# Kernel tuning notes

Measured on AMD Instinct MI355X. Metric: run time of the kernel, lower is better.

The kernel has to match this reference:

```python
import jax, jax.numpy as jnp
import numpy as np

INV_SQRT2 = 0.7071067811865476  # Haar (db1) filter coefficient


def haar_dwt(x):
    """Single-level Haar DWT along last axis (even length). Matches pywt db1."""
    e = x[..., 0::2]
    o = x[..., 1::2]
    ca = (e + o) * INV_SQRT2
    cd = (e - o) * INV_SQRT2
    return ca, cd


def haar_idwt(ca, cd):
    """Single-level Haar inverse DWT along last axis. Matches pywt waverec."""
    e = (ca + cd) * INV_SQRT2
    o = (ca - cd) * INV_SQRT2
    # interleave: out[2k]=e[k], out[2k+1]=o[k]
    return jnp.stack([e, o], axis=-1).reshape(ca.shape[:-1] + (2 * ca.shape[-1],))


def _soft_threshold(c, thr):
    a = jnp.abs(c)
    return jnp.where(a >= thr, jnp.sign(c) * (a - thr), jnp.zeros_like(c))


def setup_inputs() -> dict:
    key = jax.random.key(0)
    x = jax.random.normal(key, (64, 1024, 1024), dtype=jnp.float32)
    return {"x": x}


def reference(x):
    # x: [B, C, L]; 3-level Haar decomposition per (b, c) signal, vectorized.
    L = x.shape[-1]
    ca1, cd1 = haar_dwt(x)    # [B,C,L/2]
    ca2, cd2 = haar_dwt(ca1)  # [B,C,L/4]
    ca3, cd3 = haar_dwt(ca2)  # [B,C,L/8]

    # Universal threshold per signal: sigma = median(|cd1|)/0.6745,
    # lamda = sigma * sqrt(2*ln(L))  (natural log, as in math.log(L, e)).
    median_cd1 = jnp.median(jnp.abs(cd1), axis=-1, keepdims=True)  # [B,C,1]
    sigma = median_cd1 / 0.6745
    lamda = sigma * np.sqrt(2.0 * np.log(float(L))).astype(np.float32)

    # Per-level soft thresholds: lamda/log2(2), lamda/log2(3), lamda/log2(4).
    cd1 = _soft_threshold(cd1, lamda / np.float32(np.log2(2.0)))
    cd2 = _soft_threshold(cd2, lamda / np.float32(np.log2(3.0)))
    cd3 = _soft_threshold(cd3, lamda / np.float32(np.log2(4.0)))

    # Reconstruct with kept ca3 and thresholded details.
    ca2r = haar_idwt(ca3, cd3)
    ca1r = haar_idwt(ca2r, cd2)
    return haar_idwt(ca1r, cd1)
```

## Files before the change

### kernel.cpp

```cpp
#include <hip/hip_runtime.h>

#define L 1024
#define BLOCK 256

__device__ __forceinline__ float soft_thr(float c, float thr) {
    float a = fabsf(c);
    return (a >= thr) ? copysignf(a - thr, c) : 0.0f;
}

__device__ __forceinline__ int imin2(int a, int b) { return (a < b) ? a : b; }
__device__ __forceinline__ int imax2(int a, int b) { return (a > b) ? a : b; }

__global__ __launch_bounds__(BLOCK) void wavelet_denoise_kernel(
        const float* __restrict__ x, float* __restrict__ out) {
    constexpr float IS2 = 0.70710678118654752f;
    constexpr float SQRT_2LOGL = 3.7232974111f;

    const int lane = threadIdx.x & 63;
    const int wid  = threadIdx.x >> 6;
    const long long row = (long long)blockIdx.x * 4 + wid;
    const float* xr = x + row * L;
    float* orow = out + row * L;

    float4 in[4];
    #pragma unroll
    for (int j = 0; j < 4; ++j)
        in[j] = ((const float4*)xr)[j * 64 + lane];

    float ca1[8], cd1[8];
    #pragma unroll
    for (int j = 0; j < 4; ++j) {
        ca1[2*j]   = (in[j].x + in[j].y) * IS2;
        cd1[2*j]   = (in[j].x - in[j].y) * IS2;
        ca1[2*j+1] = (in[j].z + in[j].w) * IS2;
        cd1[2*j+1] = (in[j].z - in[j].w) * IS2;
    }

    float ca2[4], cd2[4];
    #pragma unroll
    for (int j = 0; j < 4; ++j) {
        ca2[j] = (ca1[2*j] + ca1[2*j+1]) * IS2;
        cd2[j] = (ca1[2*j] - ca1[2*j+1]) * IS2;
    }

    float ca3[4], cd3[4];
    #pragma unroll
    for (int j = 0; j < 4; ++j) {
        float o = __shfl_xor(ca2[j], 1);
        ca3[j] = (ca2[j] + o) * IS2;
        cd3[j] = (ca2[j] - o) * IS2;
    }

    int w[8];
    const int b0 = -(int)( lane       & 1);
    const int b1 = -(int)((lane >> 1) & 1);
    const int b2 = -(int)((lane >> 2) & 1);
    const int b3 = -(int)((lane >> 3) & 1);
    const int b4 = -(int)((lane >> 4) & 1);
    const int b5 = -(int)((lane >> 5) & 1);

    #pragma unroll
    for (int r = 0; r < 8; ++r)
        w[r] = (__float_as_int(cd1[r]) & 0x7fffffff) ^ b0;

    #define CE(a, c) { int _lo = imin2(w[a], w[c]); int _hi = imax2(w[a], w[c]); \
                       w[a] = _lo; w[c] = _hi; }

    CE(0,1) CE(2,3) CE(4,5) CE(6,7)
    CE(0,2) CE(1,3) CE(4,6) CE(5,7)
    CE(1,2) CE(5,6)
    CE(0,4) CE(1,5) CE(2,6) CE(3,7)
    CE(2,4) CE(3,5)
    CE(1,2) CE(3,4) CE(5,6)

    #define XORW(T) { const int _t = (T); \
        _Pragma("unroll") for (int r = 0; r < 8; ++r) w[r] ^= _t; }

    #define CROSS_STAGE(LM) { const bool _up = (lane & (LM)) != 0; \
        _Pragma("unroll") for (int r = 0; r < 8; ++r) { \
            int _o = __shfl_xor(w[r], (LM)); \
            w[r] = _up ? imax2(w[r], _o) : imin2(w[r], _o); } }

    #define INLANE3() { \
        CE(0,4) CE(1,5) CE(2,6) CE(3,7) \
        CE(0,2) CE(1,3) CE(4,6) CE(5,7) \
        CE(0,1) CE(2,3) CE(4,5) CE(6,7) }

    XORW(b0 ^ b1); CROSS_STAGE(1);                                                             INLANE3();
    XORW(b1 ^ b2); CROSS_STAGE(2);  CROSS_STAGE(1);                                            INLANE3();
    XORW(b2 ^ b3); CROSS_STAGE(4);  CROSS_STAGE(2); CROSS_STAGE(1);                            INLANE3();
    XORW(b3 ^ b4); CROSS_STAGE(8);  CROSS_STAGE(4); CROSS_STAGE(2); CROSS_STAGE(1);            INLANE3();
    XORW(b4 ^ b5); CROSS_STAGE(16); CROSS_STAGE(8); CROSS_STAGE(4); CROSS_STAGE(2); CROSS_STAGE(1); INLANE3();
    XORW(b5);      CROSS_STAGE(32);

    int zmx = imax2(imax2(imax2(w[0], w[1]), imax2(w[2], w[3])),
                    imax2(imax2(w[4], w[5]), imax2(w[6], w[7])));
    int zmn = imin2(imin2(imin2(w[0], w[1]), imin2(w[2], w[3])),
                    imin2(imin2(w[4], w[5]), imin2(w[6], w[7])));
    int z = (lane & 32) ? ~zmn : zmx;
    #pragma unroll
    for (int m = 1; m <= 16; m <<= 1)
        z = imax2(z, __shfl_xor(z, m));
    const float m0 = __int_as_float(__shfl(z, 0));
    const float m1 = __int_as_float(~__shfl(z, 32));

    #undef CE
    #undef XORW
    #undef CROSS_STAGE
    #undef INLANE3

    const float median = 0.5f * (m0 + m1);
    const float lam  = (median / 0.6745f) * SQRT_2LOGL;
    const float thr1 = lam;
    const float thr2 = lam / 1.5849625007f;
    const float thr3 = lam * 0.5f;

    #pragma unroll
    for (int j = 0; j < 4; ++j) {
        float c3 = __shfl(ca3[j], lane & 62);
        float d3 = soft_thr(__shfl(cd3[j], lane & 62), thr3);
        float ca2r = ((lane & 1) == 0) ? (c3 + d3) * IS2 : (c3 - d3) * IS2;

        float d2 = soft_thr(cd2[j], thr2);
        float ca1r0 = (ca2r + d2) * IS2;
        float ca1r1 = (ca2r - d2) * IS2;

        float d10 = soft_thr(cd1[2*j],   thr1);
        float d11 = soft_thr(cd1[2*j+1], thr1);
        float4 o;
        o.x = (ca1r0 + d10) * IS2;
        o.y = (ca1r0 - d10) * IS2;
        o.z = (ca1r1 + d11) * IS2;
        o.w = (ca1r1 - d11) * IS2;
        ((float4*)orow)[j * 64 + lane] = o;
    }
}

extern "C" void kernel_launch(void* const* d_in, const int* in_sizes, int n_in,
                              void* d_out, int out_size, void* d_ws, size_t ws_size,
                              hipStream_t stream) {
    const float* x = (const float*)d_in[0];
    float* out = (float*)d_out;
    const int rows = in_sizes[0] / L;
    wavelet_denoise_kernel<<<rows / 4, BLOCK, 0, stream>>>(x, out);
}
```

Measured before the change: 437.2 us.

## Process eight rows per wave with software-prefetched double buffering

Each wave now handles eight consecutive rows instead of one and loads the next row into a second register buffer while the current row's transform and median sort run. The aim is to hide global load latency behind the sorting-network work and cut the number of blocks launched. Launch bounds now request four blocks per CU as a minimum. The costs are higher register pressure and eight times fewer waves, which reduces the parallelism available to hide memory latency on a memory-bound kernel.

```diff
diff --git a/kernel.cpp b/kernel.cpp
--- a/kernel.cpp
+++ b/kernel.cpp
@@ -2,6 +2,7 @@
 
 #define L 1024
 #define BLOCK 256
+#define NITER 8
 
 __device__ __forceinline__ float soft_thr(float c, float thr) {
     float a = fabsf(c);
@@ -11,46 +12,7 @@
 __device__ __forceinline__ int imin2(int a, int b) { return (a < b) ? a : b; }
 __device__ __forceinline__ int imax2(int a, int b) { return (a > b) ? a : b; }
 
-__global__ __launch_bounds__(BLOCK) void wavelet_denoise_kernel(
-        const float* __restrict__ x, float* __restrict__ out) {
-    constexpr float IS2 = 0.70710678118654752f;
-    constexpr float SQRT_2LOGL = 3.7232974111f;
-
-    const int lane = threadIdx.x & 63;
-    const int wid  = threadIdx.x >> 6;
-    const long long row = (long long)blockIdx.x * 4 + wid;
-    const float* xr = x + row * L;
-    float* orow = out + row * L;
-
-    float4 in[4];
-    #pragma unroll
-    for (int j = 0; j < 4; ++j)
-        in[j] = ((const float4*)xr)[j * 64 + lane];
-
-    float ca1[8], cd1[8];
-    #pragma unroll
-    for (int j = 0; j < 4; ++j) {
-        ca1[2*j]   = (in[j].x + in[j].y) * IS2;
-        cd1[2*j]   = (in[j].x - in[j].y) * IS2;
-        ca1[2*j+1] = (in[j].z + in[j].w) * IS2;
-        cd1[2*j+1] = (in[j].z - in[j].w) * IS2;
-    }
-
-    float ca2[4], cd2[4];
-    #pragma unroll
-    for (int j = 0; j < 4; ++j) {
-        ca2[j] = (ca1[2*j] + ca1[2*j+1]) * IS2;
-        cd2[j] = (ca1[2*j] - ca1[2*j+1]) * IS2;
-    }
-
-    float ca3[4], cd3[4];
-    #pragma unroll
-    for (int j = 0; j < 4; ++j) {
-        float o = __shfl_xor(ca2[j], 1);
-        ca3[j] = (ca2[j] + o) * IS2;
-        cd3[j] = (ca2[j] - o) * IS2;
-    }
-
+__device__ __forceinline__ float median512(const float (&cd1)[8], int lane) {
     int w[8];
     const int b0 = -(int)( lane       & 1);
     const int b1 = -(int)((lane >> 1) & 1);
@@ -109,7 +71,46 @@
     #undef CROSS_STAGE
     #undef INLANE3
 
-    const float median = 0.5f * (m0 + m1);
+    return 0.5f * (m0 + m1);
+}
+
+template<bool PREF>
+__device__ __forceinline__ void process_row(const float4 (&in)[4], float4 (&pref)[4],
+        const float* __restrict__ pref_src, float* __restrict__ orow, int lane) {
+    constexpr float IS2 = 0.70710678118654752f;
+    constexpr float SQRT_2LOGL = 3.7232974111f;
+
+    float ca1[8], cd1[8];
+    #pragma unroll
+    for (int j = 0; j < 4; ++j) {
+        ca1[2*j]   = (in[j].x + in[j].y) * IS2;
+        cd1[2*j]   = (in[j].x - in[j].y) * IS2;
+        ca1[2*j+1] = (in[j].z + in[j].w) * IS2;
+        cd1[2*j+1] = (in[j].z - in[j].w) * IS2;
+    }
+
+    if (PREF) {
+        #pragma unroll
+        for (int j = 0; j < 4; ++j)
+            pref[j] = ((const float4*)pref_src)[j * 64 + lane];
+    }
+
+    float ca2[4], cd2[4];
+    #pragma unroll
+    for (int j = 0; j < 4; ++j) {
+        ca2[j] = (ca1[2*j] + ca1[2*j+1]) * IS2;
+        cd2[j] = (ca1[2*j] - ca1[2*j+1]) * IS2;
+    }
+
+    float ca3[4], cd3[4];
+    #pragma unroll
+    for (int j = 0; j < 4; ++j) {
+        float o = __shfl_xor(ca2[j], 1);
+        ca3[j] = (ca2[j] + o) * IS2;
+        cd3[j] = (ca2[j] - o) * IS2;
+    }
+
+    const float median = median512(cd1, lane);
     const float lam  = (median / 0.6745f) * SQRT_2LOGL;
     const float thr1 = lam;
     const float thr2 = lam / 1.5849625007f;
@@ -136,11 +137,40 @@
     }
 }
 
+__global__ __launch_bounds__(BLOCK, 4) void wavelet_denoise_kernel(
+        const float* __restrict__ x, float* __restrict__ out) {
+    const int lane = threadIdx.x & 63;
+    const int wid  = threadIdx.x >> 6;
+    const long long wave = (long long)blockIdx.x * 4 + wid;
+    const long long row0 = wave * NITER;
+    const float* xr = x + row0 * L;
+    float* orow = out + row0 * L;
+
+    float4 bufA[4], bufB[4];
+    #pragma unroll
+    for (int j = 0; j < 4; ++j)
+        bufA[j] = ((const float4*)xr)[j * 64 + lane];
+
+    #pragma unroll
+    for (int it = 0; it < NITER; it += 2) {
+        process_row<true>(bufA, bufB, xr + (long long)(it + 1) * L,
+                          orow + (long long)it * L, lane);
+        if (it + 2 < NITER) {
+            process_row<true>(bufB, bufA, xr + (long long)(it + 2) * L,
+                              orow + (long long)(it + 1) * L, lane);
+        } else {
+            process_row<false>(bufB, bufA, nullptr,
+                               orow + (long long)(it + 1) * L, lane);
+        }
+    }
+}
+
 extern "C" void kernel_launch(void* const* d_in, const int* in_sizes, int n_in,
                               void* d_out, int out_size, void* d_ws, size_t ws_size,
                               hipStream_t stream) {
     const float* x = (const float*)d_in[0];
     float* out = (float*)d_out;
     const int rows = in_sizes[0] / L;
-    wavelet_denoise_kernel<<<rows / 4, BLOCK, 0, stream>>>(x, out);
+    const int blocks = rows / (4 * NITER);
+    wavelet_denoise_kernel<<<blocks, BLOCK, 0, stream>>>(x, out);
 }
```

After: 445.0 us. No clear change (+1.8%).
